# Optimization experiments

Measured on AMD Instinct MI355X. Metric: run time of the kernel, lower is better.

## Reference

```python
import jax, jax.numpy as jnp
import numpy as np

K = 8192        # nodes (radio links)
DEG = 32        # out-degree per node
E = K * DEG
GE = 8          # graph_embedding_size
VAR = np.float32((10.0 ** (-19.9) * 5e6) / 10.0)  # output_noise_power / tx_power


def _init_mlp(key, dims_list):
    # per-node stacked Linear params, torch default init U(-1/sqrt(fan_in), 1/sqrt(fan_in))
    params = []
    for (din, dout) in dims_list:
        key, k1, k2 = jax.random.split(key, 3)
        b = float(1.0 / np.sqrt(din))
        params.append(jax.random.uniform(k1, (K, din, dout), minval=-b, maxval=b, dtype=jnp.float32))
        params.append(jax.random.uniform(k2, (K, dout), minval=-b, maxval=b, dtype=jnp.float32))
    return params


def setup_inputs() -> dict:
    key = jax.random.key(0)
    k = jax.random.split(key, 8)
    # edges sorted by src, exactly DEG distinct non-self out-neighbors per node
    src = jnp.repeat(jnp.arange(K), DEG)
    gaps = jax.random.randint(k[0], (K, DEG), 1, (K - 1) // DEG + 1)
    dst = ((jnp.arange(K)[:, None] + jnp.cumsum(gaps, axis=1)) % K).reshape(-1)
    edge_index = jnp.stack([src, dst])
    x = jax.random.uniform(k[1], (K, 1 + GE), dtype=jnp.float32)
    edge_attr = jax.random.uniform(k[2], (E, 1), dtype=jnp.float32)
    H = jax.random.uniform(k[3], (K, K), dtype=jnp.float32) * 1e-12  # |h_ij|^2 gains
    Wm1, bm1, Wm2, bm2 = _init_mlp(k[4], [(2 + GE, 32), (32, 32)])
    Wu1, bu1, Wu2, bu2 = _init_mlp(k[5], [(33 + GE, 16), (16, GE)])
    Wh1, bh1, Wh2, bh2 = _init_mlp(k[6], [(GE, 16), (16, 1)])
    return dict(x=x, edge_attr=edge_attr, H=H, edge_index=edge_index,
                Wm1=Wm1, bm1=bm1, Wm2=Wm2, bm2=bm2,
                Wu1=Wu1, bu1=bu1, Wu2=Wu2, bu2=bu2,
                Wh1=Wh1, bh1=bh1, Wh2=Wh2, bh2=bh2)


def reference(x, edge_attr, H, edge_index,
              Wm1, bm1, Wm2, bm2, Wu1, bu1, Wu2, bu2, Wh1, bh1, Wh2, bh2):
    src, dst = edge_index[0], edge_index[1]

    def conv(x):
        # message: tmp_e = [x[src_e], edge_attr_e]; node src's private mlp_m.
        # edges are contiguous groups of DEG per src -> grouped GEMM as batched einsum
        tmp = jnp.concatenate([x[src], edge_attr], axis=1).reshape(K, DEG, 2 + GE)
        h = jax.nn.relu(jnp.einsum('ked,kdh->keh', tmp, Wm1) + bm1[:, None])
        msg = jax.nn.relu(jnp.einsum('ked,kdh->keh', h, Wm2) + bm2[:, None])
        aggr = msg.sum(axis=1)                                  # [K,32] sum-aggregate
        t = jnp.concatenate([x, aggr], axis=1)                  # [K,41]
        u = jax.nn.relu(jnp.einsum('kd,kdh->kh', t, Wu1) + bu1)
        comb = jax.nn.relu(jnp.einsum('kd,kdh->kh', u, Wu2) + bu2)  # [K,8]
        return jnp.concatenate([x[:, :1], comb], axis=1)        # keep direct-channel col

    x3 = conv(conv(conv(x)))                                    # 3 rounds of LocalConv
    emb = x3[:, 1:]                                             # [K,8]
    hh = jax.nn.relu(jnp.einsum('kd,kdh->kh', emb, Wh1) + bh1)
    p = jax.nn.sigmoid(jnp.einsum('kd,kdh->kh', hh, Wh2) + bh2)[:, 0]  # power in (0,1)

    # per-node (negative) local rate over 1-hop out-neighborhood
    valid = p * jnp.diagonal(H)                                 # p_i * |h_ii|^2
    interf = jax.ops.segment_sum(p[dst] * H[src, dst], src, num_segments=K) + VAR
    interf = jax.lax.stop_gradient(interf)                      # .detach() in original
    local_rate = -jnp.log2(1.0 + valid / interf)                # [K]
    return local_rate
```

## Files before the change

### kernel.cpp

```cpp
#include <hip/hip_runtime.h>
#include <hip/hip_bf16.h>
#include <math.h>

#define KN 8192
#define DEG 32
#define EE (KN*DEG)

#define VAR_F 6.294627058970831e-15f

typedef __attribute__((ext_vector_type(8)))  short bf16x8;
typedef __attribute__((ext_vector_type(16))) float f32x16;

static __device__ __forceinline__ short bf_hi(float f) {
    __hip_bfloat16 h = __float2bfloat16(f);
    return __builtin_bit_cast(short, h);
}
static __device__ __forceinline__ float bf_f(short s) {
    __hip_bfloat16 h = __builtin_bit_cast(__hip_bfloat16, s);
    return __bfloat162float(h);
}

__global__ __launch_bounds__(64, 4) void mpnn_fused(
    const float* __restrict__ x,
    const float* __restrict__ edge_attr,
    const float* __restrict__ H,
    const int* __restrict__ edge_index,
    const float* __restrict__ Wm1, const float* __restrict__ bm1,
    const float* __restrict__ Wm2, const float* __restrict__ bm2,
    const float* __restrict__ Wu1, const float* __restrict__ bu1,
    const float* __restrict__ Wu2, const float* __restrict__ bu2,
    const float* __restrict__ Wh1, const float* __restrict__ bh1,
    const float* __restrict__ Wh2, const float* __restrict__ bh2,
    float* __restrict__ p_ws, float* __restrict__ valid_ws,
    float* __restrict__ hv_ws)
{
    __shared__ __align__(16) float c_lds[32];
    __shared__ float xt[44];
    __shared__ float ubuf[16];

    const int lane = threadIdx.x;
    const int col  = lane & 31;
    const int g    = lane >> 5;
    const int k    = blockIdx.x;

    const int m  = lane & 15;
    const int dg = lane >> 4;
    const int o  = lane & 7;
    const int mg = lane >> 3;

    const int* dst = edge_index + EE;
    const int dv = dst[k*DEG + col];
    const float Hv    = H[(size_t)k*KN + dv];
    const float Hdiag = H[(size_t)k*KN + k];

    const float a_e = edge_attr[k*32 + col];

    float wm1[9];
    #pragma unroll
    for (int d = 0; d < 9; ++d) wm1[d] = Wm1[(size_t)k*320 + d*32 + col];

    float w9v[16];
    {
        const float* w9p = Wm1 + (size_t)k*320 + 288;
        float4 wa = *(const float4*)(w9p + g*8);
        float4 wb = *(const float4*)(w9p + g*8 + 4);
        float4 wc = *(const float4*)(w9p + 16 + g*8);
        float4 wd = *(const float4*)(w9p + 16 + g*8 + 4);
        w9v[0]=wa.x;  w9v[1]=wa.y;  w9v[2]=wa.z;  w9v[3]=wa.w;
        w9v[4]=wb.x;  w9v[5]=wb.y;  w9v[6]=wb.z;  w9v[7]=wb.w;
        w9v[8]=wc.x;  w9v[9]=wc.y;  w9v[10]=wc.z; w9v[11]=wc.w;
        w9v[12]=wd.x; w9v[13]=wd.y; w9v[14]=wd.z; w9v[15]=wd.w;
    }

    float wm2f[16];
    #pragma unroll
    for (int s = 0; s < 2; ++s)
        #pragma unroll
        for (int i = 0; i < 8; ++i)
            wm2f[s*8+i] = Wm2[(size_t)k*1024 + (s*16 + g*8 + i)*32 + col];

    const float bm1_i = bm1[k*32 + col];
    const float bm2_i = bm2[k*32 + col];

    float wu1[11];
    #pragma unroll
    for (int t = 0; t < 11; ++t) {
        int d = dg*11 + t;
        wu1[t] = (d < 41) ? Wu1[(size_t)k*656 + d*16 + m] : 0.f;
    }
    const float bu1_m = bu1[k*16 + m];

    const float wu2a  = Wu2[(size_t)k*128 + (mg*2+0)*8 + o];
    const float wu2b  = Wu2[(size_t)k*128 + (mg*2+1)*8 + o];
    const float bu2_o = bu2[k*8 + o];

    float wh1[8];
    #pragma unroll
    for (int d = 0; d < 8; ++d) wh1[d] = Wh1[(size_t)k*128 + d*16 + m];
    const float bh1_m = bh1[k*16 + m];
    const float wh2_m = Wh2[k*16 + m];
    const float bh2_k = bh2[k];

    if (lane < 9) xt[lane] = x[(size_t)k*9 + lane];

    if (g == 0) hv_ws[k*DEG + col] = Hv;

    bf16x8 Bhi[2], Blo[2];
    #pragma unroll
    for (int s = 0; s < 2; ++s) {
        #pragma unroll
        for (int i = 0; i < 8; ++i) {
            float wv = wm2f[s*8+i];
            short h = bf_hi(wv);
            Bhi[s][i] = h;
            Blo[s][i] = bf_hi(wv - bf_f(h));
        }
    }

    for (int it = 0; it < 3; ++it) {
        float c = bm1_i;
        #pragma unroll
        for (int d = 0; d < 9; ++d) c = fmaf(xt[d], wm1[d], c);
        if (g == 0) c_lds[col] = c;

        const float4* cb = (const float4*)c_lds;
        float4 q0 = cb[g*2 + 0];
        float4 q1 = cb[g*2 + 1];
        float4 q2 = cb[4 + g*2 + 0];
        float4 q3 = cb[4 + g*2 + 1];
        float cv[16] = {q0.x,q0.y,q0.z,q0.w, q1.x,q1.y,q1.z,q1.w,
                        q2.x,q2.y,q2.z,q2.w, q3.x,q3.y,q3.z,q3.w};
        bf16x8 Ahi[2], Alo[2];
        #pragma unroll
        for (int s = 0; s < 2; ++s) {
            #pragma unroll
            for (int i = 0; i < 8; ++i) {
                int t = s*8 + i;
                float hv = fmaxf(fmaf(a_e, w9v[t], cv[t]), 0.f);
                short h = bf_hi(hv);
                Ahi[s][i] = h;
                Alo[s][i] = bf_hi(hv - bf_f(h));
            }
        }

        f32x16 acc;
        #pragma unroll
        for (int r = 0; r < 16; ++r) acc[r] = 0.f;
        #pragma unroll
        for (int s = 0; s < 2; ++s) {
            acc = __builtin_amdgcn_mfma_f32_32x32x16_bf16(Ahi[s], Bhi[s], acc, 0, 0, 0);
            acc = __builtin_amdgcn_mfma_f32_32x32x16_bf16(Ahi[s], Blo[s], acc, 0, 0, 0);
            acc = __builtin_amdgcn_mfma_f32_32x32x16_bf16(Alo[s], Bhi[s], acc, 0, 0, 0);
        }

        float ag = 0.f;
        #pragma unroll
        for (int r = 0; r < 16; ++r) ag += fmaxf(acc[r] + bm2_i, 0.f);
        ag += __shfl_xor(ag, 32);
        if (g == 0) xt[9 + col] = ag;

        float up = 0.f;
        #pragma unroll
        for (int t = 0; t < 11; ++t) {
            int d = dg*11 + t;
            if (d < 41) up = fmaf(xt[d], wu1[t], up);
        }
        up += __shfl_xor(up, 16);
        up += __shfl_xor(up, 32);
        float u = fmaxf(up + bu1_m, 0.f);
        if (lane < 16) ubuf[lane] = u;

        float cp = wu2a * ubuf[mg*2] + wu2b * ubuf[mg*2 + 1];
        cp += __shfl_xor(cp, 8);
        cp += __shfl_xor(cp, 16);
        cp += __shfl_xor(cp, 32);
        float comb = fmaxf(cp + bu2_o, 0.f);
        if (lane < 8) xt[1 + lane] = comb;
    }

    float hp = 0.f;
    #pragma unroll
    for (int d = 0; d < 8; ++d) hp = fmaf(xt[1 + d], wh1[d], hp);
    float hh = fmaxf(hp + bh1_m, 0.f);
    float pp = hh * wh2_m;
    pp += __shfl_xor(pp, 1);
    pp += __shfl_xor(pp, 2);
    pp += __shfl_xor(pp, 4);
    pp += __shfl_xor(pp, 8);
    float z = pp + bh2_k;
    float p = 1.f / (1.f + expf(-z));
    if (lane == 0) {
        p_ws[k] = p;
        valid_ws[k] = p * Hdiag;
    }
}

__global__ __launch_bounds__(256) void mpnn_interf(
    const int* __restrict__ edge_index,
    const float* __restrict__ p_ws,
    const float* __restrict__ valid_ws,
    const float* __restrict__ hv_ws,
    float* __restrict__ out)
{
    const int t = blockIdx.x * 256 + threadIdx.x;
    const int s = t >> 5;
    const int e = t & 31;
    const int* dst = edge_index + EE;
    const int d = dst[s*DEG + e];
    float part = p_ws[d] * hv_ws[s*DEG + e];
    part += __shfl_xor(part, 1);
    part += __shfl_xor(part, 2);
    part += __shfl_xor(part, 4);
    part += __shfl_xor(part, 8);
    part += __shfl_xor(part, 16);
    if (e == 0) {
        float interf = part + VAR_F;
        out[s] = -log1pf(valid_ws[s] / interf) * 1.4426950408889634f;
    }
}

extern "C" void kernel_launch(void* const* d_in, const int* in_sizes, int n_in,
                              void* d_out, int out_size, void* d_ws, size_t ws_size,
                              hipStream_t stream) {
    const float* x         = (const float*)d_in[0];
    const float* edge_attr = (const float*)d_in[1];
    const float* H         = (const float*)d_in[2];
    const int*   edge_idx  = (const int*)  d_in[3];
    const float* Wm1 = (const float*)d_in[4];
    const float* bm1 = (const float*)d_in[5];
    const float* Wm2 = (const float*)d_in[6];
    const float* bm2 = (const float*)d_in[7];
    const float* Wu1 = (const float*)d_in[8];
    const float* bu1 = (const float*)d_in[9];
    const float* Wu2 = (const float*)d_in[10];
    const float* bu2 = (const float*)d_in[11];
    const float* Wh1 = (const float*)d_in[12];
    const float* bh1 = (const float*)d_in[13];
    const float* Wh2 = (const float*)d_in[14];
    const float* bh2 = (const float*)d_in[15];
    float* out = (float*)d_out;

    float* p_ws     = (float*)d_ws;
    float* valid_ws = p_ws + KN;
    float* hv_ws    = valid_ws + KN;

    mpnn_fused<<<KN, 64, 0, stream>>>(x, edge_attr, H, edge_idx,
                                      Wm1, bm1, Wm2, bm2,
                                      Wu1, bu1, Wu2, bu2, Wh1, bh1, Wh2, bh2,
                                      p_ws, valid_ws, hv_ws);
    mpnn_interf<<<(KN*DEG)/256, 256, 0, stream>>>(edge_idx, p_ws, valid_ws,
                                                  hv_ws, out);
}
```

Before: 30.97 us.

## Process four nodes per block with double-buffered register prefetch of weights

Each block now handles four nodes sequentially, and the per-node weights and inputs are loaded into a register struct one or two nodes ahead of the node being computed. This is meant to hide global memory latency of the per-node weight loads behind the serial compute chain of the previous node. In exchange, register pressure roughly doubles (launch bounds lowered to 2 waves), the grid shrinks fourfold, and the LDS scratch is reused across nodes without explicit barriers. That reuse is safe only because the block is a single wavefront.

```diff
diff --git a/kernel.cpp b/kernel.cpp
--- a/kernel.cpp
+++ b/kernel.cpp
@@ -20,7 +20,22 @@
     return __bfloat162float(h);
 }
 
-__global__ __launch_bounds__(64, 4) void mpnn_fused(
+struct RawW {
+    float a_e;
+    float wm1[9];
+    float w9v[16];
+    float wm2f[16];
+    float bm1_i, bm2_i;
+    float wu1[11];
+    float bu1_m, wu2a, wu2b, bu2_o;
+    float wh1[8];
+    float bh1_m, wh2_m, bh2_k;
+    float x9;
+    float Hv, Hdiag;
+    int   dv;
+};
+
+__global__ __launch_bounds__(64, 2) void mpnn_fused(
     const float* __restrict__ x,
     const float* __restrict__ edge_attr,
     const float* __restrict__ H,
@@ -41,158 +56,169 @@
     const int lane = threadIdx.x;
     const int col  = lane & 31;
     const int g    = lane >> 5;
-    const int k    = blockIdx.x;
-
-    const int m  = lane & 15;
-    const int dg = lane >> 4;
-    const int o  = lane & 7;
-    const int mg = lane >> 3;
-
-    const int* dst = edge_index + EE;
-    const int dv = dst[k*DEG + col];
-    const float Hv    = H[(size_t)k*KN + dv];
-    const float Hdiag = H[(size_t)k*KN + k];
-
-    const float a_e = edge_attr[k*32 + col];
-
-    float wm1[9];
-    #pragma unroll
-    for (int d = 0; d < 9; ++d) wm1[d] = Wm1[(size_t)k*320 + d*32 + col];
-
-    float w9v[16];
-    {
-        const float* w9p = Wm1 + (size_t)k*320 + 288;
-        float4 wa = *(const float4*)(w9p + g*8);
-        float4 wb = *(const float4*)(w9p + g*8 + 4);
-        float4 wc = *(const float4*)(w9p + 16 + g*8);
-        float4 wd = *(const float4*)(w9p + 16 + g*8 + 4);
-        w9v[0]=wa.x;  w9v[1]=wa.y;  w9v[2]=wa.z;  w9v[3]=wa.w;
-        w9v[4]=wb.x;  w9v[5]=wb.y;  w9v[6]=wb.z;  w9v[7]=wb.w;
-        w9v[8]=wc.x;  w9v[9]=wc.y;  w9v[10]=wc.z; w9v[11]=wc.w;
-        w9v[12]=wd.x; w9v[13]=wd.y; w9v[14]=wd.z; w9v[15]=wd.w;
-    }
-
-    float wm2f[16];
-    #pragma unroll
-    for (int s = 0; s < 2; ++s)
-        #pragma unroll
-        for (int i = 0; i < 8; ++i)
-            wm2f[s*8+i] = Wm2[(size_t)k*1024 + (s*16 + g*8 + i)*32 + col];
-
-    const float bm1_i = bm1[k*32 + col];
-    const float bm2_i = bm2[k*32 + col];
-
-    float wu1[11];
-    #pragma unroll
-    for (int t = 0; t < 11; ++t) {
-        int d = dg*11 + t;
-        wu1[t] = (d < 41) ? Wu1[(size_t)k*656 + d*16 + m] : 0.f;
-    }
-    const float bu1_m = bu1[k*16 + m];
-
-    const float wu2a  = Wu2[(size_t)k*128 + (mg*2+0)*8 + o];
-    const float wu2b  = Wu2[(size_t)k*128 + (mg*2+1)*8 + o];
-    const float bu2_o = bu2[k*8 + o];
-
-    float wh1[8];
-    #pragma unroll
-    for (int d = 0; d < 8; ++d) wh1[d] = Wh1[(size_t)k*128 + d*16 + m];
-    const float bh1_m = bh1[k*16 + m];
-    const float wh2_m = Wh2[k*16 + m];
-    const float bh2_k = bh2[k];
-
-    if (lane < 9) xt[lane] = x[(size_t)k*9 + lane];
-
-    if (g == 0) hv_ws[k*DEG + col] = Hv;
-
-    bf16x8 Bhi[2], Blo[2];
-    #pragma unroll
-    for (int s = 0; s < 2; ++s) {
-        #pragma unroll
-        for (int i = 0; i < 8; ++i) {
-            float wv = wm2f[s*8+i];
-            short h = bf_hi(wv);
-            Bhi[s][i] = h;
-            Blo[s][i] = bf_hi(wv - bf_f(h));
-        }
-    }
-
-    for (int it = 0; it < 3; ++it) {
-        float c = bm1_i;
-        #pragma unroll
-        for (int d = 0; d < 9; ++d) c = fmaf(xt[d], wm1[d], c);
-        if (g == 0) c_lds[col] = c;
-
-        const float4* cb = (const float4*)c_lds;
-        float4 q0 = cb[g*2 + 0];
-        float4 q1 = cb[g*2 + 1];
-        float4 q2 = cb[4 + g*2 + 0];
-        float4 q3 = cb[4 + g*2 + 1];
-        float cv[16] = {q0.x,q0.y,q0.z,q0.w, q1.x,q1.y,q1.z,q1.w,
-                        q2.x,q2.y,q2.z,q2.w, q3.x,q3.y,q3.z,q3.w};
-        bf16x8 Ahi[2], Alo[2];
-        #pragma unroll
-        for (int s = 0; s < 2; ++s) {
-            #pragma unroll
-            for (int i = 0; i < 8; ++i) {
-                int t = s*8 + i;
-                float hv = fmaxf(fmaf(a_e, w9v[t], cv[t]), 0.f);
-                short h = bf_hi(hv);
-                Ahi[s][i] = h;
-                Alo[s][i] = bf_hi(hv - bf_f(h));
-            }
-        }
-
-        f32x16 acc;
-        #pragma unroll
-        for (int r = 0; r < 16; ++r) acc[r] = 0.f;
-        #pragma unroll
-        for (int s = 0; s < 2; ++s) {
-            acc = __builtin_amdgcn_mfma_f32_32x32x16_bf16(Ahi[s], Bhi[s], acc, 0, 0, 0);
-            acc = __builtin_amdgcn_mfma_f32_32x32x16_bf16(Ahi[s], Blo[s], acc, 0, 0, 0);
-            acc = __builtin_amdgcn_mfma_f32_32x32x16_bf16(Alo[s], Bhi[s], acc, 0, 0, 0);
-        }
-
-        float ag = 0.f;
-        #pragma unroll
-        for (int r = 0; r < 16; ++r) ag += fmaxf(acc[r] + bm2_i, 0.f);
-        ag += __shfl_xor(ag, 32);
-        if (g == 0) xt[9 + col] = ag;
-
-        float up = 0.f;
+    const int m    = lane & 15;
+    const int dg   = lane >> 4;
+    const int o    = lane & 7;
+    const int mg   = lane >> 3;
+
+    const int* dstp = edge_index + EE;
+
+    auto load_raw = [&](RawW& r, int k) {
+        r.dv  = dstp[k*DEG + col];
+        r.a_e = edge_attr[k*32 + col];
+
+        #pragma unroll
+        for (int d = 0; d < 9; ++d) r.wm1[d] = Wm1[(size_t)k*320 + d*32 + col];
+
+        {
+            const float* w9p = Wm1 + (size_t)k*320 + 288;
+            float4 wa = *(const float4*)(w9p + g*8);
+            float4 wb = *(const float4*)(w9p + g*8 + 4);
+            float4 wc = *(const float4*)(w9p + 16 + g*8);
+            float4 wd = *(const float4*)(w9p + 16 + g*8 + 4);
+            r.w9v[0]=wa.x;  r.w9v[1]=wa.y;  r.w9v[2]=wa.z;  r.w9v[3]=wa.w;
+            r.w9v[4]=wb.x;  r.w9v[5]=wb.y;  r.w9v[6]=wb.z;  r.w9v[7]=wb.w;
+            r.w9v[8]=wc.x;  r.w9v[9]=wc.y;  r.w9v[10]=wc.z; r.w9v[11]=wc.w;
+            r.w9v[12]=wd.x; r.w9v[13]=wd.y; r.w9v[14]=wd.z; r.w9v[15]=wd.w;
+        }
+
+        #pragma unroll
+        for (int s = 0; s < 2; ++s)
+            #pragma unroll
+            for (int i = 0; i < 8; ++i)
+                r.wm2f[s*8+i] = Wm2[(size_t)k*1024 + (s*16 + g*8 + i)*32 + col];
+
+        r.bm1_i = bm1[k*32 + col];
+        r.bm2_i = bm2[k*32 + col];
+
         #pragma unroll
         for (int t = 0; t < 11; ++t) {
             int d = dg*11 + t;
-            if (d < 41) up = fmaf(xt[d], wu1[t], up);
-        }
-        up += __shfl_xor(up, 16);
-        up += __shfl_xor(up, 32);
-        float u = fmaxf(up + bu1_m, 0.f);
-        if (lane < 16) ubuf[lane] = u;
-
-        float cp = wu2a * ubuf[mg*2] + wu2b * ubuf[mg*2 + 1];
-        cp += __shfl_xor(cp, 8);
-        cp += __shfl_xor(cp, 16);
-        cp += __shfl_xor(cp, 32);
-        float comb = fmaxf(cp + bu2_o, 0.f);
-        if (lane < 8) xt[1 + lane] = comb;
-    }
-
-    float hp = 0.f;
-    #pragma unroll
-    for (int d = 0; d < 8; ++d) hp = fmaf(xt[1 + d], wh1[d], hp);
-    float hh = fmaxf(hp + bh1_m, 0.f);
-    float pp = hh * wh2_m;
-    pp += __shfl_xor(pp, 1);
-    pp += __shfl_xor(pp, 2);
-    pp += __shfl_xor(pp, 4);
-    pp += __shfl_xor(pp, 8);
-    float z = pp + bh2_k;
-    float p = 1.f / (1.f + expf(-z));
-    if (lane == 0) {
-        p_ws[k] = p;
-        valid_ws[k] = p * Hdiag;
-    }
+            r.wu1[t] = (d < 41) ? Wu1[(size_t)k*656 + d*16 + m] : 0.f;
+        }
+        r.bu1_m = bu1[k*16 + m];
+
+        r.wu2a  = Wu2[(size_t)k*128 + (mg*2+0)*8 + o];
+        r.wu2b  = Wu2[(size_t)k*128 + (mg*2+1)*8 + o];
+        r.bu2_o = bu2[k*8 + o];
+
+        #pragma unroll
+        for (int d = 0; d < 8; ++d) r.wh1[d] = Wh1[(size_t)k*128 + d*16 + m];
+        r.bh1_m = bh1[k*16 + m];
+        r.wh2_m = Wh2[k*16 + m];
+        r.bh2_k = bh2[k];
+
+        r.x9 = x[(size_t)k*9 + (lane < 9 ? lane : 0)];
+
+        r.Hdiag = H[(size_t)k*KN + k];
+        r.Hv    = H[(size_t)k*KN + r.dv];
+    };
+
+    auto compute_node = [&](RawW& r, int k) {
+        if (lane < 9) xt[lane] = r.x9;
+
+        bf16x8 Bhi[2], Blo[2];
+        #pragma unroll
+        for (int s = 0; s < 2; ++s) {
+            #pragma unroll
+            for (int i = 0; i < 8; ++i) {
+                float wv = r.wm2f[s*8+i];
+                short h = bf_hi(wv);
+                Bhi[s][i] = h;
+                Blo[s][i] = bf_hi(wv - bf_f(h));
+            }
+        }
+
+        for (int it = 0; it < 3; ++it) {
+            float c = r.bm1_i;
+            #pragma unroll
+            for (int d = 0; d < 9; ++d) c = fmaf(xt[d], r.wm1[d], c);
+            if (g == 0) c_lds[col] = c;
+
+            const float4* cb = (const float4*)c_lds;
+            float4 q0 = cb[g*2 + 0];
+            float4 q1 = cb[g*2 + 1];
+            float4 q2 = cb[4 + g*2 + 0];
+            float4 q3 = cb[4 + g*2 + 1];
+            float cv[16] = {q0.x,q0.y,q0.z,q0.w, q1.x,q1.y,q1.z,q1.w,
+                            q2.x,q2.y,q2.z,q2.w, q3.x,q3.y,q3.z,q3.w};
+            bf16x8 Ahi[2], Alo[2];
+            #pragma unroll
+            for (int s = 0; s < 2; ++s) {
+                #pragma unroll
+                for (int i = 0; i < 8; ++i) {
+                    int t = s*8 + i;
+                    float hv = fmaxf(fmaf(r.a_e, r.w9v[t], cv[t]), 0.f);
+                    short h = bf_hi(hv);
+                    Ahi[s][i] = h;
+                    Alo[s][i] = bf_hi(hv - bf_f(h));
+                }
+            }
+
+            f32x16 acc;
+            #pragma unroll
+            for (int rr = 0; rr < 16; ++rr) acc[rr] = 0.f;
+            #pragma unroll
+            for (int s = 0; s < 2; ++s) {
+                acc = __builtin_amdgcn_mfma_f32_32x32x16_bf16(Ahi[s], Bhi[s], acc, 0, 0, 0);
+                acc = __builtin_amdgcn_mfma_f32_32x32x16_bf16(Ahi[s], Blo[s], acc, 0, 0, 0);
+                acc = __builtin_amdgcn_mfma_f32_32x32x16_bf16(Alo[s], Bhi[s], acc, 0, 0, 0);
+            }
+
+            float ag = 0.f;
+            #pragma unroll
+            for (int rr = 0; rr < 16; ++rr) ag += fmaxf(acc[rr] + r.bm2_i, 0.f);
+            ag += __shfl_xor(ag, 32);
+            if (g == 0) xt[9 + col] = ag;
+
+            float up = 0.f;
+            #pragma unroll
+            for (int t = 0; t < 11; ++t) {
+                int d = dg*11 + t;
+                if (d < 41) up = fmaf(xt[d], r.wu1[t], up);
+            }
+            up += __shfl_xor(up, 16);
+            up += __shfl_xor(up, 32);
+            float u = fmaxf(up + r.bu1_m, 0.f);
+            if (lane < 16) ubuf[lane] = u;
+
+            float cp = r.wu2a * ubuf[mg*2] + r.wu2b * ubuf[mg*2 + 1];
+            cp += __shfl_xor(cp, 8);
+            cp += __shfl_xor(cp, 16);
+            cp += __shfl_xor(cp, 32);
+            float comb = fmaxf(cp + r.bu2_o, 0.f);
+            if (lane < 8) xt[1 + lane] = comb;
+        }
+
+        float hp = 0.f;
+        #pragma unroll
+        for (int d = 0; d < 8; ++d) hp = fmaf(xt[1 + d], r.wh1[d], hp);
+        float hh = fmaxf(hp + r.bh1_m, 0.f);
+        float pp = hh * r.wh2_m;
+        pp += __shfl_xor(pp, 1);
+        pp += __shfl_xor(pp, 2);
+        pp += __shfl_xor(pp, 4);
+        pp += __shfl_xor(pp, 8);
+        float z = pp + r.bh2_k;
+        float p = 1.f / (1.f + expf(-z));
+
+        if (g == 0) hv_ws[k*DEG + col] = r.Hv;
+        if (lane == 0) {
+            p_ws[k] = p;
+            valid_ws[k] = p * r.Hdiag;
+        }
+    };
+
+    const int k0 = blockIdx.x * 4;
+    RawW A, B;
+    load_raw(A, k0 + 0);
+    load_raw(B, k0 + 1);
+    compute_node(A, k0 + 0);
+    load_raw(A, k0 + 2);
+    compute_node(B, k0 + 1);
+    load_raw(B, k0 + 3);
+    compute_node(A, k0 + 2);
+    compute_node(B, k0 + 3);
 }
 
 __global__ __launch_bounds__(256) void mpnn_interf(
@@ -244,10 +270,10 @@
     float* valid_ws = p_ws + KN;
     float* hv_ws    = valid_ws + KN;
 
-    mpnn_fused<<<KN, 64, 0, stream>>>(x, edge_attr, H, edge_idx,
-                                      Wm1, bm1, Wm2, bm2,
-                                      Wu1, bu1, Wu2, bu2, Wh1, bh1, Wh2, bh2,
-                                      p_ws, valid_ws, hv_ws);
+    mpnn_fused<<<KN/4, 64, 0, stream>>>(x, edge_attr, H, edge_idx,
+                                        Wm1, bm1, Wm2, bm2,
+                                        Wu1, bu1, Wu2, bu2, Wh1, bh1, Wh2, bh2,
+                                        p_ws, valid_ws, hv_ws);
     mpnn_interf<<<(KN*DEG)/256, 256, 0, stream>>>(edge_idx, p_ws, valid_ws,
                                                   hv_ws, out);
 }
```

Measured after the change: 35.25 us. 13.8% more time.

## Coalesce per-node weight loads across all lanes and vectorize interference gather

Applied to the files above, without the earlier changes.

The fused kernel now loads the Wm1, Wu1 and Wh1 weight matrices with contiguous 64-lane reads, so each lane holds fewer registers. The small matvecs are split across lane groups and combined with cross-lane shuffles instead of each lane reading a strided column. The interference kernel now processes 4 edges per thread with int4/float4 loads, using 8 threads per node instead of 32. It also writes an unused Hdiag copy into the workspace, which enlarges the workspace layout. The intent is fewer load instructions and lower register pressure, at the cost of extra shuffles.

```diff
diff --git a/kernel.cpp b/kernel.cpp
--- a/kernel.cpp
+++ b/kernel.cpp
@@ -48,16 +48,16 @@
     const int o  = lane & 7;
     const int mg = lane >> 3;
 
-    const int* dst = edge_index + EE;
-    const int dv = dst[k*DEG + col];
+    const int* dstp = edge_index + EE;
+    const int dv = dstp[k*DEG + col];
     const float Hv    = H[(size_t)k*KN + dv];
     const float Hdiag = H[(size_t)k*KN + k];
 
     const float a_e = edge_attr[k*32 + col];
 
-    float wm1[9];
-    #pragma unroll
-    for (int d = 0; d < 9; ++d) wm1[d] = Wm1[(size_t)k*320 + d*32 + col];
+    float wm1v[5];
+    #pragma unroll
+    for (int t = 0; t < 5; ++t) wm1v[t] = Wm1[(size_t)k*320 + t*64 + lane];
 
     float w9v[16];
     {
@@ -82,21 +82,20 @@
     const float bm1_i = bm1[k*32 + col];
     const float bm2_i = bm2[k*32 + col];
 
-    float wu1[11];
-    #pragma unroll
-    for (int t = 0; t < 11; ++t) {
-        int d = dg*11 + t;
-        wu1[t] = (d < 41) ? Wu1[(size_t)k*656 + d*16 + m] : 0.f;
-    }
+    float wu1v[10];
+    #pragma unroll
+    for (int t = 0; t < 10; ++t) wu1v[t] = Wu1[(size_t)k*656 + t*64 + lane];
+    float wu1t = 0.f;
+    if (lane < 16) wu1t = Wu1[(size_t)k*656 + 640 + lane];
     const float bu1_m = bu1[k*16 + m];
 
     const float wu2a  = Wu2[(size_t)k*128 + (mg*2+0)*8 + o];
     const float wu2b  = Wu2[(size_t)k*128 + (mg*2+1)*8 + o];
     const float bu2_o = bu2[k*8 + o];
 
-    float wh1[8];
-    #pragma unroll
-    for (int d = 0; d < 8; ++d) wh1[d] = Wh1[(size_t)k*128 + d*16 + m];
+    float wh1v[2];
+    #pragma unroll
+    for (int t = 0; t < 2; ++t) wh1v[t] = Wh1[(size_t)k*128 + t*64 + lane];
     const float bh1_m = bh1[k*16 + m];
     const float wh2_m = Wh2[k*16 + m];
     const float bh2_k = bh2[k];
@@ -104,6 +103,7 @@
     if (lane < 9) xt[lane] = x[(size_t)k*9 + lane];
 
     if (g == 0) hv_ws[k*DEG + col] = Hv;
+    if (lane == 0) valid_ws[KN + k] = Hdiag;
 
     bf16x8 Bhi[2], Blo[2];
     #pragma unroll
@@ -118,9 +118,11 @@
     }
 
     for (int it = 0; it < 3; ++it) {
-        float c = bm1_i;
-        #pragma unroll
-        for (int d = 0; d < 9; ++d) c = fmaf(xt[d], wm1[d], c);
+        float cpart = 0.f;
+        #pragma unroll
+        for (int t = 0; t < 4; ++t) cpart = fmaf(xt[2*t + g], wm1v[t], cpart);
+        if (g == 0) cpart = fmaf(xt[8], wm1v[4], cpart);
+        float c = bm1_i + cpart + __shfl_xor(cpart, 32);
         if (g == 0) c_lds[col] = c;
 
         const float4* cb = (const float4*)c_lds;
@@ -145,7 +147,7 @@
 
         f32x16 acc;
         #pragma unroll
-        for (int r = 0; r < 16; ++r) acc[r] = 0.f;
+        for (int rr = 0; rr < 16; ++rr) acc[rr] = 0.f;
         #pragma unroll
         for (int s = 0; s < 2; ++s) {
             acc = __builtin_amdgcn_mfma_f32_32x32x16_bf16(Ahi[s], Bhi[s], acc, 0, 0, 0);
@@ -155,16 +157,14 @@
 
         float ag = 0.f;
         #pragma unroll
-        for (int r = 0; r < 16; ++r) ag += fmaxf(acc[r] + bm2_i, 0.f);
+        for (int rr = 0; rr < 16; ++rr) ag += fmaxf(acc[rr] + bm2_i, 0.f);
         ag += __shfl_xor(ag, 32);
         if (g == 0) xt[9 + col] = ag;
 
         float up = 0.f;
         #pragma unroll
-        for (int t = 0; t < 11; ++t) {
-            int d = dg*11 + t;
-            if (d < 41) up = fmaf(xt[d], wu1[t], up);
-        }
+        for (int t = 0; t < 10; ++t) up = fmaf(xt[4*t + dg], wu1v[t], up);
+        up = fmaf(xt[40], wu1t, up);
         up += __shfl_xor(up, 16);
         up += __shfl_xor(up, 32);
         float u = fmaxf(up + bu1_m, 0.f);
@@ -178,9 +178,10 @@
         if (lane < 8) xt[1 + lane] = comb;
     }
 
-    float hp = 0.f;
-    #pragma unroll
-    for (int d = 0; d < 8; ++d) hp = fmaf(xt[1 + d], wh1[d], hp);
+    float hp = fmaf(xt[1 + dg], wh1v[0], 0.f);
+    hp = fmaf(xt[1 + 4 + dg], wh1v[1], hp);
+    hp += __shfl_xor(hp, 16);
+    hp += __shfl_xor(hp, 32);
     float hh = fmaxf(hp + bh1_m, 0.f);
     float pp = hh * wh2_m;
     pp += __shfl_xor(pp, 1);
@@ -202,18 +203,19 @@
     const float* __restrict__ hv_ws,
     float* __restrict__ out)
 {
-    const int t = blockIdx.x * 256 + threadIdx.x;
-    const int s = t >> 5;
-    const int e = t & 31;
-    const int* dst = edge_index + EE;
-    const int d = dst[s*DEG + e];
-    float part = p_ws[d] * hv_ws[s*DEG + e];
+    const int tid = threadIdx.x;
+    const int s   = blockIdx.x * 32 + (tid >> 3);
+    const int e4  = tid & 7;
+    const int* dstp = edge_index + EE;
+
+    int4   d4 = ((const int4*)  (dstp  + s*DEG))[e4];
+    float4 h4 = ((const float4*)(hv_ws + s*DEG))[e4];
+    float part = p_ws[d4.x] * h4.x + p_ws[d4.y] * h4.y
+               + p_ws[d4.z] * h4.z + p_ws[d4.w] * h4.w;
     part += __shfl_xor(part, 1);
     part += __shfl_xor(part, 2);
     part += __shfl_xor(part, 4);
-    part += __shfl_xor(part, 8);
-    part += __shfl_xor(part, 16);
-    if (e == 0) {
+    if (e4 == 0) {
         float interf = part + VAR_F;
         out[s] = -log1pf(valid_ws[s] / interf) * 1.4426950408889634f;
     }
@@ -242,12 +244,12 @@
 
     float* p_ws     = (float*)d_ws;
     float* valid_ws = p_ws + KN;
-    float* hv_ws    = valid_ws + KN;
+    float* hv_ws    = valid_ws + 2*KN;
 
     mpnn_fused<<<KN, 64, 0, stream>>>(x, edge_attr, H, edge_idx,
                                       Wm1, bm1, Wm2, bm2,
                                       Wu1, bu1, Wu2, bu2, Wh1, bh1, Wh2, bh2,
                                       p_ws, valid_ws, hv_ws);
-    mpnn_interf<<<(KN*DEG)/256, 256, 0, stream>>>(edge_idx, p_ws, valid_ws,
-                                                  hv_ws, out);
-}
+    mpnn_interf<<<KN/32, 256, 0, stream>>>(edge_idx, p_ws, valid_ws,
+                                           hv_ws, out);
+}
```

New measurement: 29.93 us. 3.4% less time.
